# Kernel tuning notes

Hardware: AMD Instinct MI355X
Metric: run time of the kernel (lower is better)

## Reference

```python
import jax, jax.numpy as jnp
import numpy as np

N = 20000      # total nodes (1000 graphs x 20 nodes)
E = 160000     # total edges (avg degree 8)
B = 1000       # number of graphs
H = 2          # attention heads
C = 128        # out_channels per head (encoder_hidden)
D = H * C      # 256, node feature dim between layers
EMB = 64       # embed_dim / LSTM hidden
V = 5          # vocab
T = 21         # max_length decode steps
SOS = 1        # NT2IDX['U']
SQRT_C = float(np.sqrt(C))


def setup_inputs() -> dict:
    key = jax.random.key(0)
    ks = jax.random.split(key, 40)
    rn = lambda k, shape, s=0.05: (jax.random.normal(k, shape) * s).astype(jnp.float32)
    p = {}
    p['x'] = jax.random.normal(ks[0], (N, 4), jnp.float32)
    p['edge_index'] = jax.random.randint(ks[1], (2, E), 0, N)
    p['batch'] = jnp.repeat(jnp.arange(B), N // B)  # contiguous graph ids, all graphs nonempty
    p['gc_content'] = jax.random.uniform(ks[2], (B,), jnp.float32)
    p['seq_length'] = jnp.full((B,), 21.0, jnp.float32)
    # layer 0 TransformerConv (in=4 -> heads*C=256)
    p['c0_wq'] = rn(ks[3], (4, D)); p['c0_bq'] = rn(ks[4], (D,))
    p['c0_wk'] = rn(ks[5], (4, D)); p['c0_bk'] = rn(ks[6], (D,))
    p['c0_wv'] = rn(ks[7], (4, D)); p['c0_bv'] = rn(ks[8], (D,))
    p['c0_ws'] = rn(ks[9], (4, D)); p['c0_bs'] = rn(ks[10], (D,))
    # layers 1..2 stacked (in=256 -> 256)
    p['cw_q'] = rn(ks[11], (2, D, D)); p['cb_q'] = rn(ks[12], (2, D))
    p['cw_k'] = rn(ks[13], (2, D, D)); p['cb_k'] = rn(ks[14], (2, D))
    p['cw_v'] = rn(ks[15], (2, D, D)); p['cb_v'] = rn(ks[16], (2, D))
    p['cw_s'] = rn(ks[17], (2, D, D)); p['cb_s'] = rn(ks[18], (2, D))
    p['ln_g'] = jnp.ones((3, D), jnp.float32)
    p['ln_b'] = jnp.zeros((3, D), jnp.float32)
    p['enc_w'] = rn(ks[19], (D + 2, EMB)); p['enc_b'] = rn(ks[20], (EMB,))
    p['emb'] = rn(ks[21], (V, EMB), 1.0)
    p['w_ih'] = rn(ks[22], (EMB, 4 * EMB)); p['w_hh'] = rn(ks[23], (EMB, 4 * EMB))
    p['b_ih'] = rn(ks[24], (4 * EMB,)); p['b_hh'] = rn(ks[25], (4 * EMB,))
    p['fc_w'] = rn(ks[26], (EMB, V)); p['fc_b'] = rn(ks[27], (V,))
    return p


def _transformer_conv(x, src, tgt, wq, bq, wk, bk, wv, bv, ws, bs):
    # PyG TransformerConv, heads=H, concat=True, root_weight=True, no edge_attr.
    n = x.shape[0]
    q = (x @ wq + bq).reshape(n, H, C)[tgt]   # [E,H,C] query at target nodes
    k = (x @ wk + bk).reshape(n, H, C)[src]   # [E,H,C] key at source nodes
    v = (x @ wv + bv).reshape(n, H, C)[src]   # [E,H,C] value at source nodes
    score = (q * k).sum(-1) / SQRT_C          # [E,H]
    m = jax.ops.segment_max(score, tgt, num_segments=n)   # scatter-softmax (stable)
    a = jnp.exp(score - m[tgt])
    den = jax.ops.segment_sum(a, tgt, num_segments=n)
    alpha = a / den[tgt]                      # [E,H]
    out = jax.ops.segment_sum(alpha[..., None] * v, tgt, num_segments=n)  # [N,H,C]
    return out.reshape(n, D) + x @ ws + bs    # concat heads + skip (lin_skip)


def _layer_norm(x, g, b):
    mu = x.mean(-1, keepdims=True)
    var = ((x - mu) ** 2).mean(-1, keepdims=True)
    return (x - mu) * jax.lax.rsqrt(var + 1e-5) * g + b


def reference(x, edge_index, batch, gc_content, seq_length,
              c0_wq, c0_bq, c0_wk, c0_bk, c0_wv, c0_bv, c0_ws, c0_bs,
              cw_q, cb_q, cw_k, cb_k, cw_v, cb_v, cw_s, cb_s,
              ln_g, ln_b, enc_w, enc_b, emb, w_ih, w_hh, b_ih, b_hh, fc_w, fc_b):
    src, tgt = edge_index[0], edge_index[1]
    # ---- encoder: 3 TransformerConv + ReLU + LayerNorm (dropout=eval/identity) ----
    h = _transformer_conv(x, src, tgt, c0_wq, c0_bq, c0_wk, c0_bk, c0_wv, c0_bv, c0_ws, c0_bs)
    h = _layer_norm(jax.nn.relu(h), ln_g[0], ln_b[0])
    for i in range(2):
        h = _transformer_conv(h, src, tgt, cw_q[i], cb_q[i], cw_k[i], cb_k[i],
                              cw_v[i], cb_v[i], cw_s[i], cb_s[i])
        h = _layer_norm(jax.nn.relu(h), ln_g[i + 1], ln_b[i + 1])
    # ---- global mean pool per graph ----
    counts = jax.ops.segment_sum(jnp.ones((h.shape[0],), h.dtype), batch, num_segments=B)
    pool = jax.ops.segment_sum(h, batch, num_segments=B) / jnp.maximum(counts, 1.0)[:, None]
    gfeat = jnp.concatenate([pool, gc_content[:, None], seq_length[:, None]], axis=1)  # [B,258]
    enc = jax.nn.relu(gfeat @ enc_w + enc_b)  # [B,EMB]
    def step(carry, _):
        hs, cs, inp = carry
        g = inp @ w_ih + b_ih + hs @ w_hh + b_hh      # [B,4*EMB], torch gate order i,f,g,o
        i_g, f_g, g_g, o_g = jnp.split(g, 4, axis=-1)
        cs = jax.nn.sigmoid(f_g) * cs + jax.nn.sigmoid(i_g) * jnp.tanh(g_g)
        hs = jax.nn.sigmoid(o_g) * jnp.tanh(cs)
        logits = hs @ fc_w + fc_b                     # [B,V]
        tok = jnp.argmax(logits, axis=-1)
        return (hs, cs, emb[tok]), logits
    init = (enc, jnp.zeros_like(enc), jnp.broadcast_to(emb[SOS], (B, EMB)))
    _, logits = jax.lax.scan(step, init, None, length=T)  # [T,B,V]
    return jnp.transpose(logits, (1, 0, 2))               # [B,T,V]
```

## Files before the change

kernel.cpp:

```cpp
#include <hip/hip_runtime.h>
#include <math.h>

#define NN 20000
#define NNP 20096
#define NE 160000
#define NB 1000
#define EMB 64
#define NV 5
#define NT 21

typedef __attribute__((ext_vector_type(8))) short bf16x8;
typedef __attribute__((ext_vector_type(4))) float f32x4;

__device__ __forceinline__ float sigm(float x) { return 1.f / (1.f + expf(-x)); }

__device__ __forceinline__ ushort f2bf(float x) {
    unsigned u = __float_as_uint(x);
    unsigned r = (u + 0x7FFFu + ((u >> 16) & 1u)) >> 16;
    return (ushort)r;
}
__device__ __forceinline__ float bf2f(ushort h) {
    return __uint_as_float(((unsigned)h) << 16);
}

__device__ __forceinline__ void gl16(const ushort* g, ushort* l) {
    __builtin_amdgcn_global_load_lds((const __attribute__((address_space(1))) void*)g,
                                     (__attribute__((address_space(3))) void*)l, 16, 0, 0);
}

__global__ void k_fill(unsigned* p, int n, unsigned v) {
    int i = blockIdx.x * 256 + threadIdx.x;
    if (i < n) p[i] = v;
}

__global__ void k_count(const int* __restrict__ ei, int* __restrict__ deg,
                        int* __restrict__ bucket) {
    int e = blockIdx.x * 256 + threadIdx.x;
    if (e >= NE) return;
    int s = ei[e], t = ei[NE + e];
    int pos = atomicAdd(&deg[t], 1);
    if (pos < 64) bucket[(size_t)t * 64 + pos] = s;
}

__global__ void k_lin0(const float* __restrict__ x,
                       const float* __restrict__ wq, const float* __restrict__ bq,
                       const float* __restrict__ wk, const float* __restrict__ bk,
                       const float* __restrict__ wv, const float* __restrict__ bv,
                       const float* __restrict__ wss, const float* __restrict__ bss,
                       float* __restrict__ qkv, float* __restrict__ acc) {
    int idx = blockIdx.x * 256 + threadIdx.x;
    if (idx >= NN * 1024) return;
    int n = idx >> 10, j = idx & 1023;
    float x0 = x[n*4+0], x1 = x[n*4+1], x2 = x[n*4+2], x3 = x[n*4+3];
    const float* W; const float* bb; int col; float* outp;
    if (j < 256)      { W = wq;  bb = bq;  col = j;       outp = qkv + (size_t)n*768 + j; }
    else if (j < 512) { W = wk;  bb = bk;  col = j - 256; outp = qkv + (size_t)n*768 + j; }
    else if (j < 768) { W = wv;  bb = bv;  col = j - 512; outp = qkv + (size_t)n*768 + j; }
    else              { W = wss; bb = bss; col = j - 768; outp = acc + (size_t)n*256 + col; }
    float v = bb[col] + x0*W[col] + x1*W[256+col] + x2*W[512+col] + x3*W[768+col];
    *outp = v;
}

__global__ void k_convW(const float* __restrict__ cwq, const float* __restrict__ cwk,
                        const float* __restrict__ cwv, const float* __restrict__ cws,
                        ushort* __restrict__ WtHT, ushort* __restrict__ WtLT) {
    int idx = blockIdx.x * 256 + threadIdx.x;
    if (idx >= 2 * 64 * 1024) return;
    int n = idx & 1023;
    int rest = idx >> 10;
    int kq = rest & 63;
    int l = rest >> 6;
    int wsel = n >> 8, col = n & 255;
    const float* W = (wsel == 0) ? cwq : (wsel == 1) ? cwk : (wsel == 2) ? cwv : cws;
    W += (size_t)l * 65536;
    ushort hv[4], lv[4];
    #pragma unroll
    for (int i = 0; i < 4; ++i) {
        float v = W[(size_t)(kq * 4 + i) * 256 + col];
        hv[i] = f2bf(v);
        lv[i] = f2bf(v - bf2f(hv[i]));
    }
    int k0 = kq * 4;
    int kt = k0 >> 5, c = (k0 >> 3) & 3, j0 = k0 & 7;
    size_t o = ((size_t)l * 32 * 1024 + (size_t)(kt * 4 + c) * 1024 + n) * 8 + j0;
    *(ushort4*)(WtHT + o) = make_ushort4(hv[0], hv[1], hv[2], hv[3]);
    *(ushort4*)(WtLT + o) = make_ushort4(lv[0], lv[1], lv[2], lv[3]);
}

__global__ __launch_bounds__(256) void k_gemm4_mfma(
    const ushort* __restrict__ AhT, const ushort* __restrict__ AlT,
    const ushort* __restrict__ WtHT, const ushort* __restrict__ WtLT,
    const float* __restrict__ bq, const float* __restrict__ bk,
    const float* __restrict__ bv, const float* __restrict__ bs,
    float* __restrict__ qkv, float* __restrict__ acc) {
    __shared__ __align__(16) ushort SMEM[2][4][4][128][8];

    int id = blockIdx.x;
    int xcd = id & 7;
    int q8 = id >> 3;
    int s8 = q8 >> 3;
    int cblk = q8 & 7;
    int rblk = xcd + 8 * s8;
    if (rblk >= 157) return;
    int row0 = rblk * 128;
    int wsel = cblk >> 1;
    int coll = (cblk & 1) * 128;
    const float* bias; float* C; int ldc;
    if (wsel == 0)      { bias = bq; C = qkv;       ldc = 768; }
    else if (wsel == 1) { bias = bk; C = qkv + 256; ldc = 768; }
    else if (wsel == 2) { bias = bv; C = qkv + 512; ldc = 768; }
    else                { bias = bs; C = acc;       ldc = 256; }
    int ncol0 = cblk * 128;

    int tid = threadIdx.x;
    int w = tid >> 6, lane = tid & 63;
    int wr = w >> 1, wc = w & 1;
    int g = lane >> 4, r16 = lane & 15;

    const ushort* srcp; int rbase, rstr;
    if (w == 0)      { srcp = AhT;  rbase = row0;  rstr = NNP; }
    else if (w == 1) { srcp = AlT;  rbase = row0;  rstr = NNP; }
    else if (w == 2) { srcp = WtHT; rbase = ncol0; rstr = 1024; }
    else             { srcp = WtLT; rbase = ncol0; rstr = 1024; }
    ushort* lb0 = &SMEM[0][w][0][0][0];
    ushort* lb1 = &SMEM[1][w][0][0][0];

    f32x4 accv[4][4];
    f32x4 zz = {0.f, 0.f, 0.f, 0.f};
    #pragma unroll
    for (int m = 0; m < 4; ++m)
        #pragma unroll
        for (int n = 0; n < 4; ++n) accv[m][n] = zz;

    auto stage = [&](ushort* lb, int kt) {
        #pragma unroll
        for (int i = 0; i < 8; ++i) {
            gl16(srcp + ((size_t)((kt * 4 + (i >> 1)) * rstr + rbase + (i & 1) * 64 + lane)) * 8,
                 lb + i * 512);
        }
    };

    stage(lb0, 0);
    for (int kt = 0; kt < 8; ++kt) {
        int cur = kt & 1;
        if (kt < 7) {
            stage(cur ? lb0 : lb1, kt + 1);
            asm volatile("s_waitcnt vmcnt(8)" ::: "memory");
        } else {
            asm volatile("s_waitcnt vmcnt(0)" ::: "memory");
        }
        __builtin_amdgcn_sched_barrier(0);
        __builtin_amdgcn_s_barrier();

        bf16x8 bH[4], bL[4];
        #pragma unroll
        for (int n = 0; n < 4; ++n) {
            int rw = wc * 64 + n * 16 + r16;
            bH[n] = *(const bf16x8*)&SMEM[cur][2][g][rw][0];
            bL[n] = *(const bf16x8*)&SMEM[cur][3][g][rw][0];
        }
        #pragma unroll
        for (int m = 0; m < 4; ++m) {
            int rw = wr * 64 + m * 16 + r16;
            bf16x8 aH = *(const bf16x8*)&SMEM[cur][0][g][rw][0];
            bf16x8 aL = *(const bf16x8*)&SMEM[cur][1][g][rw][0];
            #pragma unroll
            for (int n = 0; n < 4; ++n) {
                accv[m][n] = __builtin_amdgcn_mfma_f32_16x16x32_bf16(aH, bH[n], accv[m][n], 0, 0, 0);
                accv[m][n] = __builtin_amdgcn_mfma_f32_16x16x32_bf16(aH, bL[n], accv[m][n], 0, 0, 0);
                accv[m][n] = __builtin_amdgcn_mfma_f32_16x16x32_bf16(aL, bH[n], accv[m][n], 0, 0, 0);
            }
        }
        __builtin_amdgcn_s_barrier();
    }

    float* sl = (float*)&SMEM[0][0][0][0][0] + w * 1088;
    int erow = lane >> 2;
    int ecb  = (lane & 3) * 16;
    #pragma unroll
    for (int m = 0; m < 4; ++m) {
        #pragma unroll
        for (int n = 0; n < 4; ++n) {
            int cl = coll + wc * 64 + n * 16 + r16;
            float bvv = bias[cl];
            #pragma unroll
            for (int r = 0; r < 4; ++r)
                sl[(g * 4 + r) * 68 + n * 16 + r16] = accv[m][n][r] + bvv;
        }
        int grow = row0 + wr * 64 + m * 16 + erow;
        if (grow < NN) {
            float4 v0 = *(float4*)&sl[erow * 68 + ecb + 0];
            float4 v1 = *(float4*)&sl[erow * 68 + ecb + 4];
            float4 v2 = *(float4*)&sl[erow * 68 + ecb + 8];
            float4 v3 = *(float4*)&sl[erow * 68 + ecb + 12];
            float* cp = C + (size_t)grow * ldc + coll + wc * 64 + ecb;
            ((float4*)cp)[0] = v0; ((float4*)cp)[1] = v1;
            ((float4*)cp)[2] = v2; ((float4*)cp)[3] = v3;
        }
    }
}

__global__ __launch_bounds__(256) void k_attn(const float* __restrict__ qkv,
                                              const int* __restrict__ deg,
                                              const int* __restrict__ bucket,
                                              float* __restrict__ acc) {
    __shared__ float ssc[4][64];
    __shared__ int ssrc[4][64];
    int ws = threadIdx.x >> 6, l = threadIdx.x & 63;
    int wid = blockIdx.x * 4 + ws;
    int t = wid >> 1, h = wid & 1;
    if (t >= NN) return;
    int cnt = deg[t]; if (cnt > 64) cnt = 64;
    const int* bptr = bucket + (size_t)t * 64;
    int g = l >> 4, pos = l & 15;
    const float* qp = qkv + (size_t)t * 768 + h * 128 + pos * 8;
    float4 qa = *(const float4*)qp, qb = *(const float4*)(qp + 4);

    float m = -INFINITY, den = 0.f, o0 = 0.f, o1 = 0.f;
    for (int c0 = 0; c0 < cnt; c0 += 64) {
        int clen = cnt - c0; if (clen > 64) clen = 64;
        if (l < clen) ssrc[ws][l] = bptr[c0 + l];
        for (int e = g; e < clen; e += 4) {
            int s = ssrc[ws][e];
            const float* kp = qkv + (size_t)s * 768 + 256 + h * 128 + pos * 8;
            float4 ka = *(const float4*)kp, kb = *(const float4*)(kp + 4);
            float d = qa.x*ka.x + qa.y*ka.y + qa.z*ka.z + qa.w*ka.w
                    + qb.x*kb.x + qb.y*kb.y + qb.z*kb.z + qb.w*kb.w;
            d += __shfl_xor(d, 1); d += __shfl_xor(d, 2);
            d += __shfl_xor(d, 4); d += __shfl_xor(d, 8);
            if (pos == 0) ssc[ws][e] = d * 0.08838834764831845f;
        }
        float sv = (l < clen) ? ssc[ws][l] : -INFINITY;
        float M = sv;
        #pragma unroll
        for (int off = 32; off; off >>= 1) M = fmaxf(M, __shfl_xor(M, off));
        float wl = (l < clen) ? expf(sv - M) : 0.f;
        float D = wl;
        #pragma unroll
        for (int off = 32; off; off >>= 1) D += __shfl_xor(D, off);
        ssc[ws][l] = wl;
        float nm = fmaxf(m, M);
        float so = expf(m - nm), sn = expf(M - nm);
        den = den * so + D * sn;
        o0 *= so; o1 *= so;
        float co0 = 0.f, co1 = 0.f;
        int p = 0;
        for (; p + 4 <= clen; p += 4) {
            float a0 = ssc[ws][p],     a1 = ssc[ws][p + 1];
            float a2 = ssc[ws][p + 2], a3 = ssc[ws][p + 3];
            int s0 = ssrc[ws][p],     s1 = ssrc[ws][p + 1];
            int s2 = ssrc[ws][p + 2], s3 = ssrc[ws][p + 3];
            float2 v0 = *(const float2*)(qkv + (size_t)s0 * 768 + 512 + h * 128 + l * 2);
            float2 v1 = *(const float2*)(qkv + (size_t)s1 * 768 + 512 + h * 128 + l * 2);
            float2 v2 = *(const float2*)(qkv + (size_t)s2 * 768 + 512 + h * 128 + l * 2);
            float2 v3 = *(const float2*)(qkv + (size_t)s3 * 768 + 512 + h * 128 + l * 2);
            co0 += a0 * v0.x + a1 * v1.x + a2 * v2.x + a3 * v3.x;
            co1 += a0 * v0.y + a1 * v1.y + a2 * v2.y + a3 * v3.y;
        }
        for (; p < clen; ++p) {
            float a = ssc[ws][p];
            int s = ssrc[ws][p];
            float2 v = *(const float2*)(qkv + (size_t)s * 768 + 512 + h * 128 + l * 2);
            co0 += a * v.x; co1 += a * v.y;
        }
        o0 += co0 * sn; o1 += co1 * sn;
        m = nm;
    }
    if (den > 0.f) {
        float inv = 1.f / den;
        float* op = acc + (size_t)t * 256 + h * 128 + l * 2;
        op[0] += o0 * inv;
        op[1] += o1 * inv;
    }
}

__global__ __launch_bounds__(256) void k_reluln(const float* __restrict__ acc,
                                                const float* __restrict__ g,
                                                const float* __restrict__ bta,
                                                ushort* __restrict__ AhT,
                                                ushort* __restrict__ AlT) {
    __shared__ ushort shi[4][256], slo[4][256];
    int nodeb = blockIdx.x * 4;
    int wv = threadIdx.x >> 6, lane = threadIdx.x & 63;
    int node = nodeb + wv;
    float4 v = *(const float4*)(acc + (size_t)node * 256 + lane * 4);
    v.x = fmaxf(v.x, 0.f); v.y = fmaxf(v.y, 0.f); v.z = fmaxf(v.z, 0.f); v.w = fmaxf(v.w, 0.f);
    float sum = v.x + v.y + v.z + v.w;
    #pragma unroll
    for (int o = 32; o; o >>= 1) sum += __shfl_xor(sum, o);
    float mu = sum * (1.f / 256.f);
    float d0 = v.x - mu, d1 = v.y - mu, d2 = v.z - mu, d3 = v.w - mu;
    float sq = d0*d0 + d1*d1 + d2*d2 + d3*d3;
    #pragma unroll
    for (int o = 32; o; o >>= 1) sq += __shfl_xor(sq, o);
    float rs = rsqrtf(sq * (1.f / 256.f) + 1e-5f);
    int d = lane * 4;
    float4 gg = *(const float4*)(g + d);
    float4 bb = *(const float4*)(bta + d);
    float o0 = d0 * rs * gg.x + bb.x;
    float o1 = d1 * rs * gg.y + bb.y;
    float o2 = d2 * rs * gg.z + bb.z;
    float o3 = d3 * rs * gg.w + bb.w;
    ushort4 hv, lv;
    hv.x = f2bf(o0); lv.x = f2bf(o0 - bf2f(hv.x));
    hv.y = f2bf(o1); lv.y = f2bf(o1 - bf2f(hv.y));
    hv.z = f2bf(o2); lv.z = f2bf(o2 - bf2f(hv.z));
    hv.w = f2bf(o3); lv.w = f2bf(o3 - bf2f(hv.w));
    *(ushort4*)&shi[wv][d] = hv;
    *(ushort4*)&slo[wv][d] = lv;
    __syncthreads();
    int t = threadIdx.x;
    int region = t >> 3, sub = t & 7, nd = sub >> 1, half = (sub & 1) * 4;
    size_t o = ((size_t)region * NNP + nodeb + nd) * 8 + half;
    *(ushort4*)(AhT + o) = *(ushort4*)&shi[nd][region * 8 + half];
    *(ushort4*)(AlT + o) = *(ushort4*)&slo[nd][region * 8 + half];
}

__global__ __launch_bounds__(64) void k_poolenc(const ushort* __restrict__ AhT,
                                                const ushort* __restrict__ AlT,
                                                const float* __restrict__ gc,
                                                const float* __restrict__ seq,
                                                const float* __restrict__ ew,
                                                const float* __restrict__ eb,
                                                float* __restrict__ hs) {
    int b = blockIdx.x, j = threadIdx.x;
    __shared__ __align__(16) float pool[256];
    int r = j >> 1, j0 = (j & 1) * 4;
    float4 s4 = make_float4(0.f, 0.f, 0.f, 0.f);
    for (int n = 0; n < 20; ++n) {
        size_t o = ((size_t)r * NNP + b * 20 + n) * 8 + j0;
        ushort4 hv = *(const ushort4*)(AhT + o);
        ushort4 lv = *(const ushort4*)(AlT + o);
        s4.x += bf2f(hv.x) + bf2f(lv.x);
        s4.y += bf2f(hv.y) + bf2f(lv.y);
        s4.z += bf2f(hv.z) + bf2f(lv.z);
        s4.w += bf2f(hv.w) + bf2f(lv.w);
    }
    const float inv20 = 1.f / 20.f;
    s4.x *= inv20; s4.y *= inv20; s4.z *= inv20; s4.w *= inv20;
    *(float4*)(&pool[j * 4]) = s4;
    __syncthreads();
    float sacc = eb[j];
    for (int k = 0; k < 256; ++k) sacc += pool[k] * ew[k * 64 + j];
    sacc += gc[b] * ew[256 * 64 + j] + seq[b] * ew[257 * 64 + j];
    hs[(size_t)b * 64 + j] = fmaxf(sacc, 0.f);
}

__global__ void k_xc(const float* __restrict__ emb, const float* __restrict__ wih,
                     float* __restrict__ xc) {
    int idx = blockIdx.x * 256 + threadIdx.x;
    if (idx >= 5 * 256) return;
    int v = idx >> 8, col = idx & 255;
    float s = 0.f;
    for (int k = 0; k < 64; ++k) s += emb[v * 64 + k] * wih[k * 256 + col];
    xc[idx] = s;
}

__global__ __launch_bounds__(64, 1) void k_decode(const float* __restrict__ whh,
                                                  const float* __restrict__ bih,
                                                  const float* __restrict__ bhh,
                                                  const float* __restrict__ xc,
                                                  const float* __restrict__ fcw,
                                                  const float* __restrict__ fcb,
                                                  const float* __restrict__ hs0,
                                                  float* __restrict__ out) {
    int b = blockIdx.x;
    int j = threadIdx.x;

    float wgt[4][64];
    #pragma unroll
    for (int k = 0; k < 64; ++k) {
        #pragma unroll
        for (int g = 0; g < 4; ++g)
            wgt[g][k] = whh[k * 256 + g * 64 + j];
    }
    float bs0 = bih[0 * 64 + j] + bhh[0 * 64 + j];
    float bs1 = bih[1 * 64 + j] + bhh[1 * 64 + j];
    float bs2 = bih[2 * 64 + j] + bhh[2 * 64 + j];
    float bs3 = bih[3 * 64 + j] + bhh[3 * 64 + j];
    float xcg[5][4];
    #pragma unroll
    for (int v = 0; v < 5; ++v)
        #pragma unroll
        for (int g = 0; g < 4; ++g) xcg[v][g] = xc[v * 256 + g * 64 + j];
    float fw0 = fcw[j * 5 + 0], fw1 = fcw[j * 5 + 1], fw2 = fcw[j * 5 + 2],
          fw3 = fcw[j * 5 + 3], fw4 = fcw[j * 5 + 4];
    float fb0 = fcb[0], fb1 = fcb[1], fb2 = fcb[2], fb3 = fcb[3], fb4 = fcb[4];

    float hj = hs0[(size_t)b * 64 + j];
    float cj = 0.f;
    int tok = 1;

    for (int t = 0; t < NT; ++t) {
        float xg0, xg1, xg2, xg3;
        if (tok == 0)      { xg0 = xcg[0][0]; xg1 = xcg[0][1]; xg2 = xcg[0][2]; xg3 = xcg[0][3]; }
        else if (tok == 1) { xg0 = xcg[1][0]; xg1 = xcg[1][1]; xg2 = xcg[1][2]; xg3 = xcg[1][3]; }
        else if (tok == 2) { xg0 = xcg[2][0]; xg1 = xcg[2][1]; xg2 = xcg[2][2]; xg3 = xcg[2][3]; }
        else if (tok == 3) { xg0 = xcg[3][0]; xg1 = xcg[3][1]; xg2 = xcg[3][2]; xg3 = xcg[3][3]; }
        else               { xg0 = xcg[4][0]; xg1 = xcg[4][1]; xg2 = xcg[4][2]; xg3 = xcg[4][3]; }
        float aA0 = 0.f, aA1 = 0.f, aA2 = 0.f, aA3 = 0.f;
        float aB0 = 0.f, aB1 = 0.f, aB2 = 0.f, aB3 = 0.f;
        #pragma unroll
        for (int k = 0; k < 64; k += 2) {
            float h0 = __uint_as_float(__builtin_amdgcn_readlane(__float_as_uint(hj), k));
            float h1 = __uint_as_float(__builtin_amdgcn_readlane(__float_as_uint(hj), k + 1));
            aA0 += h0 * wgt[0][k]; aA1 += h0 * wgt[1][k];
            aA2 += h0 * wgt[2][k]; aA3 += h0 * wgt[3][k];
            aB0 += h1 * wgt[0][k + 1]; aB1 += h1 * wgt[1][k + 1];
            aB2 += h1 * wgt[2][k + 1]; aB3 += h1 * wgt[3][k + 1];
        }
        float ig = sigm(bs0 + xg0 + (aA0 + aB0));
        float fg = sigm(bs1 + xg1 + (aA1 + aB1));
        float gt = tanhf(bs2 + xg2 + (aA2 + aB2));
        float og = sigm(bs3 + xg3 + (aA3 + aB3));
        cj = fg * cj + ig * gt;
        hj = og * tanhf(cj);
        float l0 = hj * fw0, l1 = hj * fw1, l2 = hj * fw2, l3 = hj * fw3, l4 = hj * fw4;
        #pragma unroll
        for (int off = 32; off; off >>= 1) {
            l0 += __shfl_xor(l0, off); l1 += __shfl_xor(l1, off);
            l2 += __shfl_xor(l2, off); l3 += __shfl_xor(l3, off);
            l4 += __shfl_xor(l4, off);
        }
        l0 += fb0; l1 += fb1; l2 += fb2; l3 += fb3; l4 += fb4;
        int tk = 0; float bv = l0;
        if (l1 > bv) { bv = l1; tk = 1; }
        if (l2 > bv) { bv = l2; tk = 2; }
        if (l3 > bv) { bv = l3; tk = 3; }
        if (l4 > bv) { bv = l4; tk = 4; }
        tok = tk;
        if (j < 5) {
            float myl = (j == 0) ? l0 : (j == 1) ? l1 : (j == 2) ? l2 : (j == 3) ? l3 : l4;
            out[(size_t)b * (NT * NV) + t * NV + j] = myl;
        }
    }
}

extern "C" void kernel_launch(void* const* d_in, const int* in_sizes, int n_in,
                              void* d_out, int out_size, void* d_ws, size_t ws_size,
                              hipStream_t stream) {
    const float* x    = (const float*)d_in[0];
    const int*   ei   = (const int*)d_in[1];
    const float* gc   = (const float*)d_in[3];
    const float* seq  = (const float*)d_in[4];
    const float* c0wq = (const float*)d_in[5];  const float* c0bq = (const float*)d_in[6];
    const float* c0wk = (const float*)d_in[7];  const float* c0bk = (const float*)d_in[8];
    const float* c0wv = (const float*)d_in[9];  const float* c0bv = (const float*)d_in[10];
    const float* c0ws = (const float*)d_in[11]; const float* c0bs = (const float*)d_in[12];
    const float* cwq  = (const float*)d_in[13]; const float* cbq  = (const float*)d_in[14];
    const float* cwk  = (const float*)d_in[15]; const float* cbk  = (const float*)d_in[16];
    const float* cwv  = (const float*)d_in[17]; const float* cbv  = (const float*)d_in[18];
    const float* cws  = (const float*)d_in[19]; const float* cbs  = (const float*)d_in[20];
    const float* lng  = (const float*)d_in[21]; const float* lnb  = (const float*)d_in[22];
    const float* ew   = (const float*)d_in[23]; const float* eb   = (const float*)d_in[24];
    const float* emb  = (const float*)d_in[25];
    const float* wih  = (const float*)d_in[26]; const float* whh  = (const float*)d_in[27];
    const float* bih  = (const float*)d_in[28]; const float* bhh  = (const float*)d_in[29];
    const float* fcw  = (const float*)d_in[30]; const float* fcb  = (const float*)d_in[31];
    (void)in_sizes; (void)n_in; (void)out_size; (void)ws_size;

    float* wsf  = (float*)d_ws;
    float* qkv  = wsf;
    float* acc  = qkv + (size_t)NN * 768;
    ushort* AhT = (ushort*)(acc + (size_t)NN * 256);
    ushort* AlT = AhT + (size_t)32 * NNP * 8;
    ushort* WtHT = AlT + (size_t)32 * NNP * 8;
    ushort* WtLT = WtHT + 2 * 32 * 1024 * 8;
    float* xc   = (float*)(WtLT + 2 * 32 * 1024 * 8);
    float* hs   = xc + 5 * 256;
    int* deg    = (int*)(hs + (size_t)NB * 64);
    int* bucket = deg + NN;

    k_fill<<<(NN + 255) / 256, 256, 0, stream>>>((unsigned*)deg, NN, 0u);
    k_count<<<(NE + 255) / 256, 256, 0, stream>>>(ei, deg, bucket);
    k_convW<<<512, 256, 0, stream>>>(cwq, cwk, cwv, cws, WtHT, WtLT);
    k_xc<<<5, 256, 0, stream>>>(emb, wih, xc);

    for (int L = 0; L < 3; ++L) {
        if (L == 0) {
            k_lin0<<<NN * 1024 / 256, 256, 0, stream>>>(x, c0wq, c0bq, c0wk, c0bk,
                                                        c0wv, c0bv, c0ws, c0bs, qkv, acc);
        } else {
            int i = L - 1;
            k_gemm4_mfma<<<1280, 256, 0, stream>>>(AhT, AlT,
                WtHT + (size_t)i * 32 * 1024 * 8, WtLT + (size_t)i * 32 * 1024 * 8,
                cbq + i * 256, cbk + i * 256, cbv + i * 256, cbs + i * 256,
                qkv, acc);
        }
        k_attn<<<(NN * 2 + 3) / 4, 256, 0, stream>>>(qkv, deg, bucket, acc);
        k_reluln<<<NN / 4, 256, 0, stream>>>(acc, lng + L * 256, lnb + L * 256, AhT, AlT);
    }
    k_poolenc<<<NB, 64, 0, stream>>>(AhT, AlT, gc, seq, ew, eb, hs);
    k_decode<<<NB, 64, 0, stream>>>(whh, bih, bhh, xc, fcw, fcb, hs, (float*)d_out);
}
```

Measured before the change: 396.8 us.

## Rework attention kernel into register-only 8-edge chunks and precompute GEMM load pointers

The attention kernel drops its shared-memory score and source buffers. It now processes edges in chunks of 8, with 8 lanes per edge each computing a 16-wide dot product, and broadcasts the softmax weights with shuffles instead of LDS round trips. This removes LDS traffic and the serial per-edge score loop, but adds more online-softmax rescale steps for high-degree nodes and always issues 8 V loads per chunk, padding missing edges to node 0. Separately, the GEMM staging code precomputes per-lane global pointers and advances them by a fixed stride rather than recomputing addresses each k-tile.

```diff
diff --git a/kernel.cpp b/kernel.cpp
--- a/kernel.cpp
+++ b/kernel.cpp
@@ -125,6 +125,12 @@
     ushort* lb0 = &SMEM[0][w][0][0][0];
     ushort* lb1 = &SMEM[1][w][0][0][0];
 
+    const ushort* ap[8];
+    #pragma unroll
+    for (int i = 0; i < 8; ++i)
+        ap[i] = srcp + ((size_t)((i >> 1) * rstr + rbase + (i & 1) * 64 + lane)) * 8;
+    const size_t kstep = (size_t)4 * rstr * 8;
+
     f32x4 accv[4][4];
     f32x4 zz = {0.f, 0.f, 0.f, 0.f};
     #pragma unroll
@@ -132,19 +138,19 @@
         #pragma unroll
         for (int n = 0; n < 4; ++n) accv[m][n] = zz;
 
-    auto stage = [&](ushort* lb, int kt) {
+    auto stage = [&](ushort* lb) {
         #pragma unroll
         for (int i = 0; i < 8; ++i) {
-            gl16(srcp + ((size_t)((kt * 4 + (i >> 1)) * rstr + rbase + (i & 1) * 64 + lane)) * 8,
-                 lb + i * 512);
+            gl16(ap[i], lb + i * 512);
+            ap[i] += kstep;
         }
     };
 
-    stage(lb0, 0);
+    stage(lb0);
     for (int kt = 0; kt < 8; ++kt) {
         int cur = kt & 1;
         if (kt < 7) {
-            stage(cur ? lb0 : lb1, kt + 1);
+            stage(cur ? lb0 : lb1);
             asm volatile("s_waitcnt vmcnt(8)" ::: "memory");
         } else {
             asm volatile("s_waitcnt vmcnt(0)" ::: "memory");
@@ -204,64 +210,49 @@
                                               const int* __restrict__ deg,
                                               const int* __restrict__ bucket,
                                               float* __restrict__ acc) {
-    __shared__ float ssc[4][64];
-    __shared__ int ssrc[4][64];
-    int ws = threadIdx.x >> 6, l = threadIdx.x & 63;
-    int wid = blockIdx.x * 4 + ws;
+    int l = threadIdx.x & 63;
+    int wid = blockIdx.x * 4 + (threadIdx.x >> 6);
     int t = wid >> 1, h = wid & 1;
     if (t >= NN) return;
     int cnt = deg[t]; if (cnt > 64) cnt = 64;
     const int* bptr = bucket + (size_t)t * 64;
-    int g = l >> 4, pos = l & 15;
-    const float* qp = qkv + (size_t)t * 768 + h * 128 + pos * 8;
-    float4 qa = *(const float4*)qp, qb = *(const float4*)(qp + 4);
+    int eg = l >> 3, sub = l & 7;
+    const float4* qp = (const float4*)(qkv + (size_t)t * 768 + h * 128 + sub * 16);
+    float4 q0 = qp[0], q1 = qp[1], q2 = qp[2], q3 = qp[3];
 
     float m = -INFINITY, den = 0.f, o0 = 0.f, o1 = 0.f;
-    for (int c0 = 0; c0 < cnt; c0 += 64) {
-        int clen = cnt - c0; if (clen > 64) clen = 64;
-        if (l < clen) ssrc[ws][l] = bptr[c0 + l];
-        for (int e = g; e < clen; e += 4) {
-            int s = ssrc[ws][e];
-            const float* kp = qkv + (size_t)s * 768 + 256 + h * 128 + pos * 8;
-            float4 ka = *(const float4*)kp, kb = *(const float4*)(kp + 4);
-            float d = qa.x*ka.x + qa.y*ka.y + qa.z*ka.z + qa.w*ka.w
-                    + qb.x*kb.x + qb.y*kb.y + qb.z*kb.z + qb.w*kb.w;
-            d += __shfl_xor(d, 1); d += __shfl_xor(d, 2);
-            d += __shfl_xor(d, 4); d += __shfl_xor(d, 8);
-            if (pos == 0) ssc[ws][e] = d * 0.08838834764831845f;
-        }
-        float sv = (l < clen) ? ssc[ws][l] : -INFINITY;
+    for (int c0 = 0; c0 < cnt; c0 += 8) {
+        int clen = cnt - c0; if (clen > 8) clen = 8;
+        float sv = -INFINITY;
+        if (eg < clen) {
+            int se = bptr[c0 + eg];
+            const float4* kp = (const float4*)(qkv + (size_t)se * 768 + 256 + h * 128 + sub * 16);
+            float4 k0 = kp[0], k1 = kp[1], k2 = kp[2], k3 = kp[3];
+            float d = q0.x*k0.x + q0.y*k0.y + q0.z*k0.z + q0.w*k0.w
+                    + q1.x*k1.x + q1.y*k1.y + q1.z*k1.z + q1.w*k1.w
+                    + q2.x*k2.x + q2.y*k2.y + q2.z*k2.z + q2.w*k2.w
+                    + q3.x*k3.x + q3.y*k3.y + q3.z*k3.z + q3.w*k3.w;
+            d += __shfl_xor(d, 1); d += __shfl_xor(d, 2); d += __shfl_xor(d, 4);
+            sv = d * 0.08838834764831845f;
+        }
         float M = sv;
-        #pragma unroll
-        for (int off = 32; off; off >>= 1) M = fmaxf(M, __shfl_xor(M, off));
-        float wl = (l < clen) ? expf(sv - M) : 0.f;
+        M = fmaxf(M, __shfl_xor(M, 8));
+        M = fmaxf(M, __shfl_xor(M, 16));
+        M = fmaxf(M, __shfl_xor(M, 32));
+        float wl = (eg < clen) ? expf(sv - M) : 0.f;
         float D = wl;
-        #pragma unroll
-        for (int off = 32; off; off >>= 1) D += __shfl_xor(D, off);
-        ssc[ws][l] = wl;
+        D += __shfl_xor(D, 8); D += __shfl_xor(D, 16); D += __shfl_xor(D, 32);
         float nm = fmaxf(m, M);
         float so = expf(m - nm), sn = expf(M - nm);
         den = den * so + D * sn;
         o0 *= so; o1 *= so;
         float co0 = 0.f, co1 = 0.f;
-        int p = 0;
-        for (; p + 4 <= clen; p += 4) {
-            float a0 = ssc[ws][p],     a1 = ssc[ws][p + 1];
-            float a2 = ssc[ws][p + 2], a3 = ssc[ws][p + 3];
-            int s0 = ssrc[ws][p],     s1 = ssrc[ws][p + 1];
-            int s2 = ssrc[ws][p + 2], s3 = ssrc[ws][p + 3];
-            float2 v0 = *(const float2*)(qkv + (size_t)s0 * 768 + 512 + h * 128 + l * 2);
-            float2 v1 = *(const float2*)(qkv + (size_t)s1 * 768 + 512 + h * 128 + l * 2);
-            float2 v2 = *(const float2*)(qkv + (size_t)s2 * 768 + 512 + h * 128 + l * 2);
-            float2 v3 = *(const float2*)(qkv + (size_t)s3 * 768 + 512 + h * 128 + l * 2);
-            co0 += a0 * v0.x + a1 * v1.x + a2 * v2.x + a3 * v3.x;
-            co1 += a0 * v0.y + a1 * v1.y + a2 * v2.y + a3 * v3.y;
-        }
-        for (; p < clen; ++p) {
-            float a = ssc[ws][p];
-            int s = ssrc[ws][p];
-            float2 v = *(const float2*)(qkv + (size_t)s * 768 + 512 + h * 128 + l * 2);
-            co0 += a * v.x; co1 += a * v.y;
+        #pragma unroll
+        for (int k = 0; k < 8; ++k) {
+            int sk = (k < clen) ? bptr[c0 + k] : 0;
+            float ak = __shfl(wl, k * 8);
+            float2 v = *(const float2*)(qkv + (size_t)sk * 768 + 512 + h * 128 + l * 2);
+            co0 += ak * v.x; co1 += ak * v.y;
         }
         o0 += co0 * sn; o1 += co1 * sn;
         m = nm;
```

New measurement: 450.8 us. 1.14x slower.

## Fuse attention aggregation with residual ReLU LayerNorm and bf16 split store

Applied to the files above, without the earlier changes.

Merges the attention kernel and the ReLU+LayerNorm kernel into one: each block handles two nodes (two heads each), adds the skip term, applies ReLU into shared memory, and then two waves do LayerNorm and write the hi/lo bf16 transposed layout directly. This removes a kernel launch and the read-modify-write round trip of the acc buffer per layer. It also precomputes the GEMM staging pointers and advances them incrementally instead of recomputing addresses each k-step. The LN phase uses only half the waves, and the uncoalesced transposed stores are now scattered per node.

```diff
diff --git a/kernel.cpp b/kernel.cpp
--- a/kernel.cpp
+++ b/kernel.cpp
@@ -125,6 +125,12 @@
     ushort* lb0 = &SMEM[0][w][0][0][0];
     ushort* lb1 = &SMEM[1][w][0][0][0];
 
+    const ushort* ap[8];
+    #pragma unroll
+    for (int i = 0; i < 8; ++i)
+        ap[i] = srcp + ((size_t)((i >> 1) * rstr + rbase + (i & 1) * 64 + lane)) * 8;
+    const size_t kstep = (size_t)4 * rstr * 8;
+
     f32x4 accv[4][4];
     f32x4 zz = {0.f, 0.f, 0.f, 0.f};
     #pragma unroll
@@ -132,19 +138,19 @@
         #pragma unroll
         for (int n = 0; n < 4; ++n) accv[m][n] = zz;
 
-    auto stage = [&](ushort* lb, int kt) {
+    auto stage = [&](ushort* lb) {
         #pragma unroll
         for (int i = 0; i < 8; ++i) {
-            gl16(srcp + ((size_t)((kt * 4 + (i >> 1)) * rstr + rbase + (i & 1) * 64 + lane)) * 8,
-                 lb + i * 512);
+            gl16(ap[i], lb + i * 512);
+            ap[i] += kstep;
         }
     };
 
-    stage(lb0, 0);
+    stage(lb0);
     for (int kt = 0; kt < 8; ++kt) {
         int cur = kt & 1;
         if (kt < 7) {
-            stage(cur ? lb0 : lb1, kt + 1);
+            stage(cur ? lb0 : lb1);
             asm volatile("s_waitcnt vmcnt(8)" ::: "memory");
         } else {
             asm volatile("s_waitcnt vmcnt(0)" ::: "memory");
@@ -200,19 +206,23 @@
     }
 }
 
-__global__ __launch_bounds__(256) void k_attn(const float* __restrict__ qkv,
-                                              const int* __restrict__ deg,
-                                              const int* __restrict__ bucket,
-                                              float* __restrict__ acc) {
+__global__ __launch_bounds__(256) void k_attn_ln(const float* __restrict__ qkv,
+                                                 const int* __restrict__ deg,
+                                                 const int* __restrict__ bucket,
+                                                 const float* __restrict__ acc,
+                                                 const float* __restrict__ lg,
+                                                 const float* __restrict__ lb,
+                                                 ushort* __restrict__ AhT,
+                                                 ushort* __restrict__ AlT) {
     __shared__ float ssc[4][64];
     __shared__ int ssrc[4][64];
+    __shared__ __align__(16) float srow[2][256];
     int ws = threadIdx.x >> 6, l = threadIdx.x & 63;
-    int wid = blockIdx.x * 4 + ws;
-    int t = wid >> 1, h = wid & 1;
-    if (t >= NN) return;
+    int t = blockIdx.x * 2 + (ws >> 1);
+    int h = ws & 1;
     int cnt = deg[t]; if (cnt > 64) cnt = 64;
     const int* bptr = bucket + (size_t)t * 64;
-    int g = l >> 4, pos = l & 15;
+    int gq = l >> 4, pos = l & 15;
     const float* qp = qkv + (size_t)t * 768 + h * 128 + pos * 8;
     float4 qa = *(const float4*)qp, qb = *(const float4*)(qp + 4);
 
@@ -220,7 +230,7 @@
     for (int c0 = 0; c0 < cnt; c0 += 64) {
         int clen = cnt - c0; if (clen > 64) clen = 64;
         if (l < clen) ssrc[ws][l] = bptr[c0 + l];
-        for (int e = g; e < clen; e += 4) {
+        for (int e = gq; e < clen; e += 4) {
             int s = ssrc[ws][e];
             const float* kp = qkv + (size_t)s * 768 + 256 + h * 128 + pos * 8;
             float4 ka = *(const float4*)kp, kb = *(const float4*)(kp + 4);
@@ -266,54 +276,40 @@
         o0 += co0 * sn; o1 += co1 * sn;
         m = nm;
     }
-    if (den > 0.f) {
-        float inv = 1.f / den;
-        float* op = acc + (size_t)t * 256 + h * 128 + l * 2;
-        op[0] += o0 * inv;
-        op[1] += o1 * inv;
-    }
-}
-
-__global__ __launch_bounds__(256) void k_reluln(const float* __restrict__ acc,
-                                                const float* __restrict__ g,
-                                                const float* __restrict__ bta,
-                                                ushort* __restrict__ AhT,
-                                                ushort* __restrict__ AlT) {
-    __shared__ ushort shi[4][256], slo[4][256];
-    int nodeb = blockIdx.x * 4;
-    int wv = threadIdx.x >> 6, lane = threadIdx.x & 63;
-    int node = nodeb + wv;
-    float4 v = *(const float4*)(acc + (size_t)node * 256 + lane * 4);
-    v.x = fmaxf(v.x, 0.f); v.y = fmaxf(v.y, 0.f); v.z = fmaxf(v.z, 0.f); v.w = fmaxf(v.w, 0.f);
-    float sum = v.x + v.y + v.z + v.w;
-    #pragma unroll
-    for (int o = 32; o; o >>= 1) sum += __shfl_xor(sum, o);
-    float mu = sum * (1.f / 256.f);
-    float d0 = v.x - mu, d1 = v.y - mu, d2 = v.z - mu, d3 = v.w - mu;
-    float sq = d0*d0 + d1*d1 + d2*d2 + d3*d3;
-    #pragma unroll
-    for (int o = 32; o; o >>= 1) sq += __shfl_xor(sq, o);
-    float rs = rsqrtf(sq * (1.f / 256.f) + 1e-5f);
-    int d = lane * 4;
-    float4 gg = *(const float4*)(g + d);
-    float4 bb = *(const float4*)(bta + d);
-    float o0 = d0 * rs * gg.x + bb.x;
-    float o1 = d1 * rs * gg.y + bb.y;
-    float o2 = d2 * rs * gg.z + bb.z;
-    float o3 = d3 * rs * gg.w + bb.w;
-    ushort4 hv, lv;
-    hv.x = f2bf(o0); lv.x = f2bf(o0 - bf2f(hv.x));
-    hv.y = f2bf(o1); lv.y = f2bf(o1 - bf2f(hv.y));
-    hv.z = f2bf(o2); lv.z = f2bf(o2 - bf2f(hv.z));
-    hv.w = f2bf(o3); lv.w = f2bf(o3 - bf2f(hv.w));
-    *(ushort4*)&shi[wv][d] = hv;
-    *(ushort4*)&slo[wv][d] = lv;
+    float inv = (den > 0.f) ? 1.f / den : 0.f;
+    float2 sk = *(const float2*)(acc + (size_t)t * 256 + h * 128 + l * 2);
+    float v0 = fmaxf(sk.x + o0 * inv, 0.f);
+    float v1 = fmaxf(sk.y + o1 * inv, 0.f);
+    *(float2*)&srow[ws >> 1][h * 128 + l * 2] = make_float2(v0, v1);
     __syncthreads();
-    int t = threadIdx.x;
-    int region = t >> 3, sub = t & 7, nd = sub >> 1, half = (sub & 1) * 4;
-    size_t o = ((size_t)region * NNP + nodeb + nd) * 8 + half;
-    *(ushort4*)(AhT + o) = *(ushort4*)&shi[nd][region * 8 + half];
-    *(ushort4*)(AlT + o) = *(ushort4*)&slo[nd][region * 8 + half];
+    if (ws < 2) {
+        int tt = blockIdx.x * 2 + ws;
+        float4 v = *(const float4*)&srow[ws][l * 4];
+        float sum = v.x + v.y + v.z + v.w;
+        #pragma unroll
+        for (int o = 32; o; o >>= 1) sum += __shfl_xor(sum, o);
+        float mu = sum * (1.f / 256.f);
+        float d0 = v.x - mu, d1 = v.y - mu, d2 = v.z - mu, d3 = v.w - mu;
+        float sq = d0*d0 + d1*d1 + d2*d2 + d3*d3;
+        #pragma unroll
+        for (int o = 32; o; o >>= 1) sq += __shfl_xor(sq, o);
+        float rs = rsqrtf(sq * (1.f / 256.f) + 1e-5f);
+        int d = l * 4;
+        float4 gg = *(const float4*)(lg + d);
+        float4 bb = *(const float4*)(lb + d);
+        float e0 = d0 * rs * gg.x + bb.x;
+        float e1 = d1 * rs * gg.y + bb.y;
+        float e2 = d2 * rs * gg.z + bb.z;
+        float e3 = d3 * rs * gg.w + bb.w;
+        ushort4 hv, lv;
+        hv.x = f2bf(e0); lv.x = f2bf(e0 - bf2f(hv.x));
+        hv.y = f2bf(e1); lv.y = f2bf(e1 - bf2f(hv.y));
+        hv.z = f2bf(e2); lv.z = f2bf(e2 - bf2f(hv.z));
+        hv.w = f2bf(e3); lv.w = f2bf(e3 - bf2f(hv.w));
+        size_t o = ((size_t)(l >> 1) * NNP + tt) * 8 + (l & 1) * 4;
+        *(ushort4*)(AhT + o) = hv;
+        *(ushort4*)(AlT + o) = lv;
+    }
 }
 
 __global__ __launch_bounds__(64) void k_poolenc(const ushort* __restrict__ AhT,
@@ -487,8 +483,8 @@
                 cbq + i * 256, cbk + i * 256, cbv + i * 256, cbs + i * 256,
                 qkv, acc);
         }
-        k_attn<<<(NN * 2 + 3) / 4, 256, 0, stream>>>(qkv, deg, bucket, acc);
-        k_reluln<<<NN / 4, 256, 0, stream>>>(acc, lng + L * 256, lnb + L * 256, AhT, AlT);
+        k_attn_ln<<<NN / 2, 256, 0, stream>>>(qkv, deg, bucket, acc,
+                                              lng + L * 256, lnb + L * 256, AhT, AlT);
     }
     k_poolenc<<<NB, 64, 0, stream>>>(AhT, AlT, gc, seq, ew, eb, hs);
     k_decode<<<NB, 64, 0, stream>>>(whh, bih, bhh, xc, fcw, fcb, hs, (float*)d_out);
```

After: 383.8 us. -3.3%, faster.
